# Performance work log

Hardware: AMD Instinct MI355X
Metric: run time of the kernel (lower is better)

## Reference

```python
import jax, jax.numpy as jnp
import numpy as np

D_MODEL = 1024
N_HEADS = 16
D_HEAD = D_MODEL // N_HEADS
D_FF = 4096
ACT_BITS = 8
GSIZE = 64
EPS = 1e-6


def act_quant(x):
    # per-group int8 activation quantization with straight-through estimator
    qmax = 2.0 ** (ACT_BITS - 1) - 1.0  # 127
    g = x.reshape(x.shape[:-1] + (-1, GSIZE))
    s = jnp.clip(jnp.max(jnp.abs(g), axis=-1, keepdims=True), 1e-5, None) / qmax
    q = jnp.clip(jnp.round(g / s), -qmax, qmax) * s
    out = g + jax.lax.stop_gradient(q - g)  # STE
    return out.reshape(x.shape)


def weight_quant_1b(w):
    # binarize to sign(w) * mean(|w|), STE
    alpha = jnp.mean(jnp.abs(w))
    wq = jnp.sign(w) * alpha
    return w + jax.lax.stop_gradient(wq - w)


def bitlinear(x, w):
    # y = Q_act(x) @ Q_w(w)^T ; w is [out, in]
    return act_quant(x) @ weight_quant_1b(w).T


def rmsnorm(x, g):
    return x * jax.lax.rsqrt(jnp.mean(x * x, axis=-1, keepdims=True) + EPS) * g


def causal_sdpa(q, k, v):
    # q,k,v: [B,H,T,Dh]
    T = q.shape[2]
    scores = jnp.einsum('bhqd,bhkd->bhqk', q, k) / jnp.sqrt(jnp.asarray(D_HEAD, q.dtype))
    mask = jnp.tril(jnp.ones((T, T), dtype=bool))
    scores = jnp.where(mask, scores, jnp.asarray(-1e30, q.dtype))
    p = jax.nn.softmax(scores, axis=-1)
    return jnp.einsum('bhqk,bhkd->bhqd', p, v)


def setup_inputs() -> dict:
    key = jax.random.key(0)
    ks = jax.random.split(key, 11)
    sd = 0.02
    inp = {
        'x': jax.random.normal(ks[0], (1, 4096, D_MODEL), dtype=jnp.float32),
        'wq': jax.random.normal(ks[1], (D_MODEL, D_MODEL), dtype=jnp.float32) * sd,
        'wk': jax.random.normal(ks[2], (D_MODEL, D_MODEL), dtype=jnp.float32) * sd,
        'wv': jax.random.normal(ks[3], (D_MODEL, D_MODEL), dtype=jnp.float32) * sd,
        'wo': jax.random.normal(ks[4], (D_MODEL, D_MODEL), dtype=jnp.float32) * sd,
        'w1': jax.random.normal(ks[5], (D_FF, D_MODEL), dtype=jnp.float32) * sd,
        'w2': jax.random.normal(ks[6], (D_FF, D_MODEL), dtype=jnp.float32) * sd,
        'w3': jax.random.normal(ks[7], (D_MODEL, D_FF), dtype=jnp.float32) * sd,
        'g1': jnp.ones((D_MODEL,), dtype=jnp.float32),
        'g2': jnp.ones((D_MODEL,), dtype=jnp.float32),
    }
    return inp


def reference(x, wq, wk, wv, wo, w1, w2, w3, g1, g2):
    B, T, C = x.shape
    # attention branch
    h = rmsnorm(x, g1)
    q = bitlinear(h, wq).reshape(B, T, N_HEADS, D_HEAD).transpose(0, 2, 1, 3)
    k = bitlinear(h, wk).reshape(B, T, N_HEADS, D_HEAD).transpose(0, 2, 1, 3)
    v = bitlinear(h, wv).reshape(B, T, N_HEADS, D_HEAD).transpose(0, 2, 1, 3)
    y = causal_sdpa(q, k, v).transpose(0, 2, 1, 3).reshape(B, T, C)
    x = x + bitlinear(y, wo)
    # SwiGLU FFN branch
    h2 = rmsnorm(x, g2)
    ff = bitlinear(jax.nn.silu(bitlinear(h2, w1)) * bitlinear(h2, w2), w3)
    return x + ff
```

## Files before the change

### kernel.cpp

```cpp
#include <hip/hip_runtime.h>
#include <math.h>


typedef unsigned short u16;
typedef __attribute__((ext_vector_type(4))) float f32x4;
typedef __attribute__((ext_vector_type(4))) unsigned short u16x4;
typedef __attribute__((ext_vector_type(8))) unsigned short u16x8;
typedef __attribute__((ext_vector_type(8))) __bf16 bf16x8;

#define DEV static __device__ __forceinline__

DEV float bf2f(u16 u) { union { unsigned i; float f; } c; c.i = ((unsigned)u) << 16; return c.f; }
DEV u16 f2bf(float f) { __bf16 b = (__bf16)f; return __builtin_bit_cast(u16, b); }

DEV void gload16(const void* g, void* l) {
  __builtin_amdgcn_global_load_lds((__attribute__((address_space(1))) void*)g,
                                   (__attribute__((address_space(3))) void*)l,
                                   16, 0, 0);
}

__global__ __launch_bounds__(256) void convert_sign_all(
    const float* __restrict__ w0, const float* __restrict__ w1,
    const float* __restrict__ w2, const float* __restrict__ w3,
    const float* __restrict__ w4, const float* __restrict__ w5,
    const float* __restrict__ w6, u16* __restrict__ sgn_base,
    float* __restrict__ partial) {
  __shared__ float red[4];
  const int wi = blockIdx.y;
  const float* srcs[7] = {w0, w1, w2, w3, w4, w5, w6};
  const size_t offs[7] = {0, 1048576, 2097152, 3145728, 4194304, 8388608, 12582912};
  const float* w = srcs[wi];
  u16* sgn = sgn_base + offs[wi];
  const int n4 = (wi < 4) ? 262144 : 1048576;

  float s = 0.f;
  for (int i = blockIdx.x * 256 + threadIdx.x; i < n4; i += 256 * 256) {
    f32x4 v = ((const f32x4*)w)[i];
    u16x4 o;
#pragma unroll
    for (int j = 0; j < 4; ++j) {
      float f = v[j];
      o[j] = f > 0.f ? (u16)0x3F80 : (f < 0.f ? (u16)0xBF80 : (u16)0);
      s += fabsf(f);
    }
    ((u16x4*)sgn)[i] = o;
  }
#pragma unroll
  for (int off = 32; off >= 1; off >>= 1) s += __shfl_xor(s, off);
  if ((threadIdx.x & 63) == 0) red[threadIdx.x >> 6] = s;
  __syncthreads();
  if (threadIdx.x == 0)
    partial[wi * 256 + blockIdx.x] = red[0] + red[1] + red[2] + red[3];
}

__global__ __launch_bounds__(256) void finalize_alpha(
    const float* __restrict__ partial, float* __restrict__ alphas) {
  __shared__ float red[4];
  int wi = blockIdx.x;
  float v = partial[wi * 256 + threadIdx.x];
#pragma unroll
  for (int off = 32; off >= 1; off >>= 1) v += __shfl_xor(v, off);
  if ((threadIdx.x & 63) == 0) red[threadIdx.x >> 6] = v;
  __syncthreads();
  if (threadIdx.x == 0)
    alphas[wi] = (red[0] + red[1] + red[2] + red[3]) *
                 (wi < 4 ? (1.f / 1048576.f) : (1.f / 4194304.f));
}

__global__ __launch_bounds__(256) void rmsnorm_quant(
    const float* __restrict__ x, const float* __restrict__ g, u16* __restrict__ out) {
  __shared__ float red[4];
  const int row = blockIdx.x, t = threadIdx.x;
  f32x4 v = ((const f32x4*)(x + (size_t)row * 1024))[t];
  float ss = v[0] * v[0] + v[1] * v[1] + v[2] * v[2] + v[3] * v[3];
#pragma unroll
  for (int off = 32; off >= 1; off >>= 1) ss += __shfl_xor(ss, off);
  if ((t & 63) == 0) red[t >> 6] = ss;
  __syncthreads();
  float tot = red[0] + red[1] + red[2] + red[3];
  float rinv = rsqrtf(tot * (1.f / 1024.f) + 1e-6f);
  f32x4 gg = ((const f32x4*)g)[t];
  float n[4];
#pragma unroll
  for (int j = 0; j < 4; ++j) n[j] = v[j] * rinv * gg[j];
  float gm = fmaxf(fmaxf(fabsf(n[0]), fabsf(n[1])), fmaxf(fabsf(n[2]), fabsf(n[3])));
#pragma unroll
  for (int off = 1; off <= 8; off <<= 1) gm = fmaxf(gm, __shfl_xor(gm, off));
  float s = fmaxf(gm, 1e-5f) / 127.0f;
  u16x4 o;
#pragma unroll
  for (int j = 0; j < 4; ++j) {
    float q = fminf(fmaxf(rintf(n[j] / s), -127.f), 127.f) * s;
    o[j] = f2bf(q);
  }
  ((u16x4*)out)[(size_t)row * 256 + t] = o;
}

__global__ __launch_bounds__(256) void silu_mul_quant(
    const u16* __restrict__ y1y2, u16* __restrict__ zq) {
  size_t idx = (size_t)blockIdx.x * 1024 + threadIdx.x * 4;
  size_t row = idx >> 12, c = idx & 4095;
  u16x4 a4 = *(const u16x4*)(y1y2 + row * 8192 + c);
  u16x4 b4 = *(const u16x4*)(y1y2 + row * 8192 + 4096 + c);
  float z[4];
#pragma unroll
  for (int j = 0; j < 4; ++j) {
    float a = bf2f(a4[j]);
    z[j] = a / (1.f + __expf(-a)) * bf2f(b4[j]);
  }
  float gm = fmaxf(fmaxf(fabsf(z[0]), fabsf(z[1])), fmaxf(fabsf(z[2]), fabsf(z[3])));
#pragma unroll
  for (int off = 1; off <= 8; off <<= 1) gm = fmaxf(gm, __shfl_xor(gm, off));
  float s = fmaxf(gm, 1e-5f) / 127.0f;
  u16x4 o;
#pragma unroll
  for (int j = 0; j < 4; ++j) {
    float q = fminf(fmaxf(rintf(z[j] / s), -127.f), 127.f) * s;
    o[j] = f2bf(q);
  }
  *(u16x4*)(zq + idx) = o;
}

__global__ __launch_bounds__(256) void transpose_v(
    const u16* __restrict__ qkv, u16* __restrict__ Vt) {
  __shared__ u16 T[64][65];
  const int tt = blockIdx.x, h = blockIdx.y, tid = threadIdx.x;
#pragma unroll
  for (int i = 0; i < 2; ++i) {
    int idx = i * 2048 + tid * 8;
    int trow = idx >> 6, dcol = idx & 63;
    u16x8 v = *(const u16x8*)(qkv + (size_t)(tt * 64 + trow) * 3072 + 2048 + h * 64 + dcol);
#pragma unroll
    for (int j = 0; j < 8; ++j) T[dcol + j][trow] = v[j];
  }
  __syncthreads();
#pragma unroll
  for (int i = 0; i < 2; ++i) {
    int idx = i * 2048 + tid * 8;
    int drow = idx >> 6, tcol = idx & 63;
    u16x8 v;
#pragma unroll
    for (int j = 0; j < 8; ++j) v[j] = T[drow][tcol + j];
    *(u16x8*)(Vt + ((size_t)h * 64 + drow) * 4096 + tt * 64 + tcol) = v;
  }
}

template <bool RES, int BM>
__global__ __launch_bounds__(256) void gemm_bt(
    const u16* __restrict__ A, const u16* __restrict__ B,
    const float* __restrict__ alpha, int ashift, const float* __restrict__ res,
    void* __restrict__ Cout, int M, int N, int K) {
  constexpr int NI = (BM == 128) ? 4 : 2;
  constexpr int WNE = (BM == 128) ? 64 : 32;
  __shared__ u16 As[BM * 64];
  __shared__ u16 Bs[128 * 64];
  const int tid = threadIdx.x;
  const int l = tid & 63, w = tid >> 6;
  const int wm = (BM == 128) ? (w >> 1) : 0;
  const int wn = (BM == 128) ? (w & 1) : w;
  const int lr = l & 15, lg = l >> 4;
  const int xorv = (l & 7) << 4;
  const int brow = blockIdx.y * BM;
  const int bcol = blockIdx.x * 128;
  const int src_chunk = (l & 7) ^ (l >> 3);
  const int rl = w * 8 + (l >> 3);

  f32x4 acc[4][NI];
#pragma unroll
  for (int i = 0; i < 4; ++i)
#pragma unroll
    for (int j = 0; j < NI; ++j) acc[i][j] = (f32x4){0.f, 0.f, 0.f, 0.f};

  const char* Ag = (const char*)A;
  const char* Bg = (const char*)B;
  const int nkt = K >> 6;
  for (int kt = 0; kt < nkt; ++kt) {
    __syncthreads();
    const size_t kb = (size_t)kt * 128 + src_chunk * 16;
#pragma unroll
    for (int it = 0; it < BM / 32; ++it)
      gload16(Ag + (size_t)(brow + it * 32 + rl) * (size_t)(K * 2) + kb,
              &As[(it * 32 + w * 8) * 64]);
#pragma unroll
    for (int it = 0; it < 4; ++it)
      gload16(Bg + (size_t)(bcol + it * 32 + rl) * (size_t)(K * 2) + kb,
              &Bs[(it * 32 + w * 8) * 64]);
    __syncthreads();

    bf16x8 af[4][2], bfr[NI][2];
#pragma unroll
    for (int mi = 0; mi < 4; ++mi)
#pragma unroll
      for (int ks = 0; ks < 2; ++ks) {
        int row = wm * 64 + mi * 16 + lr;
        af[mi][ks] = *(const bf16x8*)((const char*)As + row * 128 + ((ks * 64 + lg * 16) ^ xorv));
      }
#pragma unroll
    for (int ni = 0; ni < NI; ++ni)
#pragma unroll
      for (int ks = 0; ks < 2; ++ks) {
        int row = wn * WNE + ni * 16 + lr;
        bfr[ni][ks] = *(const bf16x8*)((const char*)Bs + row * 128 + ((ks * 64 + lg * 16) ^ xorv));
      }
#pragma unroll
    for (int ks = 0; ks < 2; ++ks)
#pragma unroll
      for (int mi = 0; mi < 4; ++mi)
#pragma unroll
        for (int ni = 0; ni < NI; ++ni)
          acc[mi][ni] = __builtin_amdgcn_mfma_f32_16x16x32_bf16(
              af[mi][ks], bfr[ni][ks], acc[mi][ni], 0, 0, 0);
  }

  const float scale = alpha[bcol >> ashift];
#pragma unroll
  for (int mi = 0; mi < 4; ++mi)
#pragma unroll
    for (int ni = 0; ni < NI; ++ni)
#pragma unroll
      for (int r = 0; r < 4; ++r) {
        int row = brow + wm * 64 + mi * 16 + lg * 4 + r;
        int col = bcol + wn * WNE + ni * 16 + lr;
        float vv = acc[mi][ni][r] * scale;
        if (RES)
          ((float*)Cout)[(size_t)row * N + col] = res[(size_t)row * N + col] + vv;
        else
          ((u16*)Cout)[(size_t)row * N + col] = f2bf(vv);
      }
}

__global__ __launch_bounds__(256) void attn_kernel(
    const u16* __restrict__ QKV, const u16* __restrict__ Vt, u16* __restrict__ Y) {
  __shared__ u16 Ks[2][64 * 64];
  __shared__ u16 Vs[2][64 * 64];
  __shared__ u16 Ps[4][16 * 64];

  const int tid = threadIdx.x;
  const int l = tid & 63, w = tid >> 6;
  const int lr = l & 15, lg = l >> 4;
  const int xorv = (l & 7) << 4;
  const int h = blockIdx.x;
  const int y = blockIdx.y;
  const int qt = (y < 32) ? y : (95 - y);
  const int src_chunk = (l & 7) ^ (l >> 3);
  const int rl = w * 8 + (l >> 3);
  const float SC = 0.18033688f;

  const int qrow0 = qt * 64 + w * 16;
  const int nkt = qt + 1;

  bf16x8 qf[2];
#pragma unroll
  for (int ks = 0; ks < 2; ++ks)
    qf[ks] = __builtin_bit_cast(
        bf16x8, *(const u16x8*)(QKV + (size_t)(qrow0 + lr) * 3072 +
                                h * 64 + ks * 32 + lg * 8));

  f32x4 O[4];
#pragma unroll
  for (int ni = 0; ni < 4; ++ni) O[ni] = (f32x4){0.f, 0.f, 0.f, 0.f};
  float m_ = -3e38f, lsum = 0.f;

  auto STAGE = [&](int buf, int kt) {
#pragma unroll
    for (int it = 0; it < 2; ++it) {
      int krow = kt * 64 + it * 32 + rl;
      gload16((const char*)QKV + ((size_t)krow * 3072 + 1024 + h * 64) * 2 + src_chunk * 16,
              &Ks[buf][(it * 32 + w * 8) * 64]);
      int drow = it * 32 + rl;
      gload16((const char*)Vt + (((size_t)h * 64 + drow) * 4096 + kt * 64) * 2 + src_chunk * 16,
              &Vs[buf][(it * 32 + w * 8) * 64]);
    }
  };

  STAGE(0, 0);
#pragma unroll 1
  for (int kt = 0; kt < nkt; ++kt) {
    const int cur = kt & 1;
    if (kt + 1 < nkt) {
      STAGE(cur ^ 1, kt + 1);
      asm volatile("s_waitcnt vmcnt(4)" ::: "memory");
    } else {
      asm volatile("s_waitcnt vmcnt(0)" ::: "memory");
    }
    __builtin_amdgcn_s_barrier();
    __builtin_amdgcn_sched_barrier(0);

    const char* kbase = (const char*)&Ks[cur][0];
    const char* vbase = (const char*)&Vs[cur][0];

    f32x4 S[4];
#pragma unroll
    for (int ni = 0; ni < 4; ++ni) {
      S[ni] = (f32x4){0.f, 0.f, 0.f, 0.f};
#pragma unroll
      for (int ks = 0; ks < 2; ++ks) {
        bf16x8 kf = *(const bf16x8*)(kbase + (ni * 16 + lr) * 128 +
                                     ((ks * 64 + lg * 16) ^ xorv));
        S[ni] = __builtin_amdgcn_mfma_f32_16x16x32_bf16(kf, qf[ks], S[ni], 0, 0, 0);
      }
    }

    const bool diag = (kt == qt);
#pragma unroll
    for (int ni = 0; ni < 4; ++ni)
#pragma unroll
      for (int r = 0; r < 4; ++r) {
        float s = S[ni][r] * SC;
        if (diag && (ni * 16 + lg * 4 + r) > (w * 16 + lr)) s = -1e30f;
        S[ni][r] = s;
      }

    float nm = -3e38f;
#pragma unroll
    for (int ni = 0; ni < 4; ++ni)
#pragma unroll
      for (int r = 0; r < 4; ++r) nm = fmaxf(nm, S[ni][r]);
    nm = fmaxf(nm, __shfl_xor(nm, 16));
    nm = fmaxf(nm, __shfl_xor(nm, 32));
    if (__ballot(nm > m_ + 8.f)) {
      float mn = fmaxf(m_, nm);
      float fac = exp2f(m_ - mn);
      m_ = mn;
      lsum *= fac;
#pragma unroll
      for (int ni = 0; ni < 4; ++ni) O[ni] *= fac;
    }
    float rs = 0.f;
#pragma unroll
    for (int ni = 0; ni < 4; ++ni)
#pragma unroll
      for (int r = 0; r < 4; ++r) {
        float pv = exp2f(S[ni][r] - m_);
        S[ni][r] = pv;
        rs += pv;
      }
    rs += __shfl_xor(rs, 16);
    rs += __shfl_xor(rs, 32);
    lsum += rs;

#pragma unroll
    for (int ni = 0; ni < 4; ++ni) {
      u16x4 pk;
#pragma unroll
      for (int r = 0; r < 4; ++r) pk[r] = f2bf(S[ni][r]);
      *(u16x4*)((char*)&Ps[w][0] + lr * 128 + ((ni * 32 + lg * 8) ^ xorv)) = pk;
    }
    bf16x8 pt[2];
#pragma unroll
    for (int ks = 0; ks < 2; ++ks)
      pt[ks] = *(const bf16x8*)((const char*)&Ps[w][0] + lr * 128 +
                                ((ks * 64 + lg * 16) ^ xorv));

#pragma unroll
    for (int ni = 0; ni < 4; ++ni) {
#pragma unroll
      for (int ks = 0; ks < 2; ++ks) {
        bf16x8 vf = *(const bf16x8*)(vbase + (ni * 16 + lr) * 128 +
                                     ((ks * 64 + lg * 16) ^ xorv));
        O[ni] = __builtin_amdgcn_mfma_f32_16x16x32_bf16(vf, pt[ks], O[ni], 0, 0, 0);
      }
    }
    asm volatile("" ::: "memory");
    __builtin_amdgcn_s_barrier();
  }

  float rinv = 1.f / lsum;
  float o[4][4];
  float gm = 0.f;
#pragma unroll
  for (int ni = 0; ni < 4; ++ni)
#pragma unroll
    for (int r = 0; r < 4; ++r) {
      o[ni][r] = O[ni][r] * rinv;
      gm = fmaxf(gm, fabsf(o[ni][r]));
    }
  gm = fmaxf(gm, __shfl_xor(gm, 16));
  gm = fmaxf(gm, __shfl_xor(gm, 32));
  float gmc = fmaxf(gm, 1e-5f);
  float s = gmc * (1.f / 127.f);
  float inv = 127.f / gmc;
#pragma unroll
  for (int ni = 0; ni < 4; ++ni) {
    u16x4 ov;
#pragma unroll
    for (int r = 0; r < 4; ++r) {
      float q = fminf(fmaxf(rintf(o[ni][r] * inv), -127.f), 127.f) * s;
      ov[r] = f2bf(q);
    }
    *(u16x4*)(Y + (size_t)(qrow0 + lr) * 1024 + h * 64 + ni * 16 + lg * 4) = ov;
  }
}

extern "C" void kernel_launch(void* const* d_in, const int* in_sizes, int n_in,
                              void* d_out, int out_size, void* d_ws, size_t ws_size,
                              hipStream_t stream) {
  const float* x  = (const float*)d_in[0];
  const float* wq = (const float*)d_in[1];
  const float* wk = (const float*)d_in[2];
  const float* wv = (const float*)d_in[3];
  const float* wo = (const float*)d_in[4];
  const float* w1 = (const float*)d_in[5];
  const float* w2 = (const float*)d_in[6];
  const float* w3 = (const float*)d_in[7];
  const float* g1 = (const float*)d_in[8];
  const float* g2 = (const float*)d_in[9];

  char* ws = (char*)d_ws;
  const size_t MB = 1024 * 1024;
  u16* sgn   = (u16*)ws;
  u16* sWq   = (u16*)(ws + 0 * MB);
  u16* sWo   = (u16*)(ws + 6 * MB);
  u16* sW1   = (u16*)(ws + 8 * MB);
  u16* sW3   = (u16*)(ws + 24 * MB);
  float* partial = (float*)(ws + 32 * MB);
  float* alphas  = (float*)(ws + 32 * MB + 16384);
  u16* Vt    = (u16*)(ws + 33 * MB);
  float* x1  = (float*)(ws + 33 * MB);
  u16* hq    = (u16*)(ws + 49 * MB);
  u16* zq    = (u16*)(ws + 49 * MB);
  u16* qkv   = (u16*)(ws + 57 * MB);
  u16* yb    = (u16*)(ws + 81 * MB);
  u16* y1y2  = (u16*)(ws + 57 * MB);

  convert_sign_all<<<dim3(256, 7), 256, 0, stream>>>(wq, wk, wv, wo, w1, w2, w3,
                                                     sgn, partial);
  finalize_alpha<<<7, 256, 0, stream>>>(partial, alphas);

  rmsnorm_quant<<<4096, 256, 0, stream>>>(x, g1, hq);
  gemm_bt<false, 128><<<dim3(24, 32), 256, 0, stream>>>(hq, sWq, alphas, 10, nullptr,
                                                        qkv, 4096, 3072, 1024);
  transpose_v<<<dim3(64, 16), 256, 0, stream>>>(qkv, Vt);
  attn_kernel<<<dim3(16, 64), 256, 0, stream>>>(qkv, Vt, yb);
  gemm_bt<true, 64><<<dim3(8, 64), 256, 0, stream>>>(yb, sWo, alphas + 3, 31, x,
                                                     x1, 4096, 1024, 1024);
  rmsnorm_quant<<<4096, 256, 0, stream>>>(x1, g2, hq);
  gemm_bt<false, 128><<<dim3(64, 32), 256, 0, stream>>>(hq, sW1, alphas + 4, 12, nullptr,
                                                        y1y2, 4096, 8192, 1024);
  silu_mul_quant<<<16384, 256, 0, stream>>>(y1y2, zq);
  gemm_bt<true, 64><<<dim3(8, 64), 256, 0, stream>>>(zq, sW3, alphas + 6, 31, x1,
                                                     (float*)d_out, 4096, 1024, 4096);
}
```

Baseline: 332.1 us.

## Fuse W1/W2 GEMM with SiLU-mul-quant epilogue; tune attention exp and priorities

Replaces the combined W1|W2 GEMM and the separate silu_mul_quant kernel with one dual-accumulator GEMM. Each block computes matching tiles of both projections and applies SiLU, the multiply and per-group int8 quantization in registers, so the bf16 y1y2 intermediate is never written to or read back from global memory. The attention kernel also switches to a raw v_exp_f32, raises wave priority around its MFMA sections, and moves causal masking into a branch taken only on the diagonal tile. The fused GEMM is not double-buffered and holds two accumulator sets, so register pressure and occupancy may suffer.

```diff
diff --git a/kernel.cpp b/kernel.cpp
--- a/kernel.cpp
+++ b/kernel.cpp
@@ -12,6 +12,7 @@
 
 DEV float bf2f(u16 u) { union { unsigned i; float f; } c; c.i = ((unsigned)u) << 16; return c.f; }
 DEV u16 f2bf(float f) { __bf16 b = (__bf16)f; return __builtin_bit_cast(u16, b); }
+DEV float fexp2(float x) { float r; asm("v_exp_f32 %0, %1" : "=v"(r) : "v"(x)); return r; }
 
 DEV void gload16(const void* g, void* l) {
   __builtin_amdgcn_global_load_lds((__attribute__((address_space(1))) void*)g,
@@ -94,31 +95,6 @@
     o[j] = f2bf(q);
   }
   ((u16x4*)out)[(size_t)row * 256 + t] = o;
-}
-
-__global__ __launch_bounds__(256) void silu_mul_quant(
-    const u16* __restrict__ y1y2, u16* __restrict__ zq) {
-  size_t idx = (size_t)blockIdx.x * 1024 + threadIdx.x * 4;
-  size_t row = idx >> 12, c = idx & 4095;
-  u16x4 a4 = *(const u16x4*)(y1y2 + row * 8192 + c);
-  u16x4 b4 = *(const u16x4*)(y1y2 + row * 8192 + 4096 + c);
-  float z[4];
-#pragma unroll
-  for (int j = 0; j < 4; ++j) {
-    float a = bf2f(a4[j]);
-    z[j] = a / (1.f + __expf(-a)) * bf2f(b4[j]);
-  }
-  float gm = fmaxf(fmaxf(fabsf(z[0]), fabsf(z[1])), fmaxf(fabsf(z[2]), fabsf(z[3])));
-#pragma unroll
-  for (int off = 1; off <= 8; off <<= 1) gm = fmaxf(gm, __shfl_xor(gm, off));
-  float s = fmaxf(gm, 1e-5f) / 127.0f;
-  u16x4 o;
-#pragma unroll
-  for (int j = 0; j < 4; ++j) {
-    float q = fminf(fmaxf(rintf(z[j] / s), -127.f), 127.f) * s;
-    o[j] = f2bf(q);
-  }
-  *(u16x4*)(zq + idx) = o;
 }
 
 __global__ __launch_bounds__(256) void transpose_v(
@@ -229,6 +205,118 @@
       }
 }
 
+__global__ __launch_bounds__(256) void gemm_ffn(
+    const u16* __restrict__ A, const u16* __restrict__ B1,
+    const u16* __restrict__ B2, const float* __restrict__ alpha2,
+    u16* __restrict__ zq) {
+  __shared__ u16 As[128 * 64];
+  __shared__ u16 B1s[128 * 64];
+  __shared__ u16 B2s[128 * 64];
+  const int tid = threadIdx.x;
+  const int l = tid & 63, w = tid >> 6;
+  const int wm = w >> 1, wn = w & 1;
+  const int lr = l & 15, lg = l >> 4;
+  const int xorv = (l & 7) << 4;
+  const int brow = blockIdx.y * 128;
+  const int bcol = blockIdx.x * 128;
+  const int src_chunk = (l & 7) ^ (l >> 3);
+  const int rl = w * 8 + (l >> 3);
+  const int K = 1024;
+
+  f32x4 acc1[4][4], acc2[4][4];
+#pragma unroll
+  for (int i = 0; i < 4; ++i)
+#pragma unroll
+    for (int j = 0; j < 4; ++j) {
+      acc1[i][j] = (f32x4){0.f, 0.f, 0.f, 0.f};
+      acc2[i][j] = (f32x4){0.f, 0.f, 0.f, 0.f};
+    }
+
+  for (int kt = 0; kt < 16; ++kt) {
+    __syncthreads();
+    const size_t kb = (size_t)kt * 128 + src_chunk * 16;
+#pragma unroll
+    for (int it = 0; it < 4; ++it) {
+      gload16((const char*)A + (size_t)(brow + it * 32 + rl) * 2048 + kb,
+              &As[(it * 32 + w * 8) * 64]);
+      gload16((const char*)B1 + (size_t)(bcol + it * 32 + rl) * 2048 + kb,
+              &B1s[(it * 32 + w * 8) * 64]);
+      gload16((const char*)B2 + (size_t)(bcol + it * 32 + rl) * 2048 + kb,
+              &B2s[(it * 32 + w * 8) * 64]);
+    }
+    __syncthreads();
+
+    bf16x8 af[4][2], bfr[4][2];
+#pragma unroll
+    for (int mi = 0; mi < 4; ++mi)
+#pragma unroll
+      for (int ks = 0; ks < 2; ++ks) {
+        int row = wm * 64 + mi * 16 + lr;
+        af[mi][ks] = *(const bf16x8*)((const char*)As + row * 128 + ((ks * 64 + lg * 16) ^ xorv));
+      }
+#pragma unroll
+    for (int ni = 0; ni < 4; ++ni)
+#pragma unroll
+      for (int ks = 0; ks < 2; ++ks) {
+        int row = wn * 64 + ni * 16 + lr;
+        bfr[ni][ks] = *(const bf16x8*)((const char*)B1s + row * 128 + ((ks * 64 + lg * 16) ^ xorv));
+      }
+#pragma unroll
+    for (int ks = 0; ks < 2; ++ks)
+#pragma unroll
+      for (int mi = 0; mi < 4; ++mi)
+#pragma unroll
+        for (int ni = 0; ni < 4; ++ni)
+          acc1[mi][ni] = __builtin_amdgcn_mfma_f32_16x16x32_bf16(
+              af[mi][ks], bfr[ni][ks], acc1[mi][ni], 0, 0, 0);
+#pragma unroll
+    for (int ni = 0; ni < 4; ++ni)
+#pragma unroll
+      for (int ks = 0; ks < 2; ++ks) {
+        int row = wn * 64 + ni * 16 + lr;
+        bfr[ni][ks] = *(const bf16x8*)((const char*)B2s + row * 128 + ((ks * 64 + lg * 16) ^ xorv));
+      }
+#pragma unroll
+    for (int ks = 0; ks < 2; ++ks)
+#pragma unroll
+      for (int mi = 0; mi < 4; ++mi)
+#pragma unroll
+        for (int ni = 0; ni < 4; ++ni)
+          acc2[mi][ni] = __builtin_amdgcn_mfma_f32_16x16x32_bf16(
+              af[mi][ks], bfr[ni][ks], acc2[mi][ni], 0, 0, 0);
+  }
+
+  const float a1 = alpha2[0], a2 = alpha2[1];
+  const float L2E = 1.4426950408889634f;
+#pragma unroll
+  for (int mi = 0; mi < 4; ++mi)
+#pragma unroll
+    for (int r = 0; r < 4; ++r) {
+      float zz[4];
+      float gm = 0.f;
+#pragma unroll
+      for (int ni = 0; ni < 4; ++ni) {
+        float y1 = acc1[mi][ni][r] * a1;
+        float y2 = acc2[mi][ni][r] * a2;
+        float sg = y1 / (1.f + fexp2(-L2E * y1));
+        zz[ni] = sg * y2;
+        gm = fmaxf(gm, fabsf(zz[ni]));
+      }
+#pragma unroll
+      for (int off = 1; off <= 8; off <<= 1) gm = fmaxf(gm, __shfl_xor(gm, off));
+      float gmc = fmaxf(gm, 1e-5f);
+      float s = gmc * (1.f / 127.f);
+      float inv = 127.f / gmc;
+      int row = brow + wm * 64 + mi * 16 + lg * 4 + r;
+#pragma unroll
+      for (int ni = 0; ni < 4; ++ni) {
+        int col = bcol + wn * 64 + ni * 16 + lr;
+        float q = fminf(fmaxf(rintf(zz[ni] * inv), -127.f), 127.f) * s;
+        zq[(size_t)row * 4096 + col] = f2bf(q);
+      }
+    }
+}
+
 __global__ __launch_bounds__(256) void attn_kernel(
     const u16* __restrict__ QKV, const u16* __restrict__ Vt, u16* __restrict__ Y) {
   __shared__ u16 Ks[2][64 * 64];
@@ -290,6 +378,7 @@
     const char* vbase = (const char*)&Vs[cur][0];
 
     f32x4 S[4];
+    __builtin_amdgcn_s_setprio(1);
 #pragma unroll
     for (int ni = 0; ni < 4; ++ni) {
       S[ni] = (f32x4){0.f, 0.f, 0.f, 0.f};
@@ -300,16 +389,19 @@
         S[ni] = __builtin_amdgcn_mfma_f32_16x16x32_bf16(kf, qf[ks], S[ni], 0, 0, 0);
       }
     }
-
-    const bool diag = (kt == qt);
+    __builtin_amdgcn_s_setprio(0);
+
 #pragma unroll
     for (int ni = 0; ni < 4; ++ni)
 #pragma unroll
-      for (int r = 0; r < 4; ++r) {
-        float s = S[ni][r] * SC;
-        if (diag && (ni * 16 + lg * 4 + r) > (w * 16 + lr)) s = -1e30f;
-        S[ni][r] = s;
-      }
+      for (int r = 0; r < 4; ++r) S[ni][r] *= SC;
+    if (kt == qt) {
+#pragma unroll
+      for (int ni = 0; ni < 4; ++ni)
+#pragma unroll
+        for (int r = 0; r < 4; ++r)
+          if ((ni * 16 + lg * 4 + r) > (w * 16 + lr)) S[ni][r] = -3e38f;
+    }
 
     float nm = -3e38f;
 #pragma unroll
@@ -320,7 +412,7 @@
     nm = fmaxf(nm, __shfl_xor(nm, 32));
     if (__ballot(nm > m_ + 8.f)) {
       float mn = fmaxf(m_, nm);
-      float fac = exp2f(m_ - mn);
+      float fac = fexp2(m_ - mn);
       m_ = mn;
       lsum *= fac;
 #pragma unroll
@@ -331,7 +423,7 @@
     for (int ni = 0; ni < 4; ++ni)
 #pragma unroll
       for (int r = 0; r < 4; ++r) {
-        float pv = exp2f(S[ni][r] - m_);
+        float pv = fexp2(S[ni][r] - m_);
         S[ni][r] = pv;
         rs += pv;
       }
@@ -352,6 +444,7 @@
       pt[ks] = *(const bf16x8*)((const char*)&Ps[w][0] + lr * 128 +
                                 ((ks * 64 + lg * 16) ^ xorv));
 
+    __builtin_amdgcn_s_setprio(1);
 #pragma unroll
     for (int ni = 0; ni < 4; ++ni) {
 #pragma unroll
@@ -361,6 +454,7 @@
         O[ni] = __builtin_amdgcn_mfma_f32_16x16x32_bf16(vf, pt[ks], O[ni], 0, 0, 0);
       }
     }
+    __builtin_amdgcn_s_setprio(0);
     asm volatile("" ::: "memory");
     __builtin_amdgcn_s_barrier();
   }
@@ -412,16 +506,16 @@
   u16* sWq   = (u16*)(ws + 0 * MB);
   u16* sWo   = (u16*)(ws + 6 * MB);
   u16* sW1   = (u16*)(ws + 8 * MB);
+  u16* sW2   = (u16*)(ws + 16 * MB);
   u16* sW3   = (u16*)(ws + 24 * MB);
   float* partial = (float*)(ws + 32 * MB);
   float* alphas  = (float*)(ws + 32 * MB + 16384);
   u16* Vt    = (u16*)(ws + 33 * MB);
   float* x1  = (float*)(ws + 33 * MB);
   u16* hq    = (u16*)(ws + 49 * MB);
-  u16* zq    = (u16*)(ws + 49 * MB);
   u16* qkv   = (u16*)(ws + 57 * MB);
   u16* yb    = (u16*)(ws + 81 * MB);
-  u16* y1y2  = (u16*)(ws + 57 * MB);
+  u16* zq    = (u16*)(ws + 57 * MB);
 
   convert_sign_all<<<dim3(256, 7), 256, 0, stream>>>(wq, wk, wv, wo, w1, w2, w3,
                                                      sgn, partial);
@@ -435,9 +529,7 @@
   gemm_bt<true, 64><<<dim3(8, 64), 256, 0, stream>>>(yb, sWo, alphas + 3, 31, x,
                                                      x1, 4096, 1024, 1024);
   rmsnorm_quant<<<4096, 256, 0, stream>>>(x1, g2, hq);
-  gemm_bt<false, 128><<<dim3(64, 32), 256, 0, stream>>>(hq, sW1, alphas + 4, 12, nullptr,
-                                                        y1y2, 4096, 8192, 1024);
-  silu_mul_quant<<<16384, 256, 0, stream>>>(y1y2, zq);
+  gemm_ffn<<<dim3(32, 32), 256, 0, stream>>>(hq, sW1, sW2, alphas + 4, zq);
   gemm_bt<true, 64><<<dim3(8, 64), 256, 0, stream>>>(zq, sW3, alphas + 6, 31, x1,
                                                      (float*)d_out, 4096, 1024, 4096);
 }
```

New measurement: 361.5 us. 8.9% more time.
